# Optimization experiments

Measured on AMD Instinct MI355X. Metric: run time of the kernel, lower is better.

The kernel has to match this reference:

```python
import jax, jax.numpy as jnp
import numpy as np

CLASS_NUM = 12
ROWS, COLS = 3, 4
ALPHA = 0.6

def _att_values():
    # attention_lst[i][j] = 1 / (# of 8-connected neighbors of cell i in the
    # ROWSxCOLS stimulus grid); note it is independent of j.
    i = np.arange(CLASS_NUM)
    r, c = i // COLS, i % COLS
    up, dn = (r - 1 >= 0), (r + 1 <= ROWS - 1)
    lf, rt = (c - 1 >= 0), (c + 1 <= COLS - 1)
    cnt = (up.astype(np.int32) + dn + lf + rt
           + (up & lf) + (up & rt) + (dn & lf) + (dn & rt))
    return (1.0 / cnt).astype(np.float32)

_ATT = jnp.asarray(_att_values())  # [CLASS_NUM]

def setup_inputs() -> dict:
    key = jax.random.key(0)
    k1, k2 = jax.random.split(key)
    B = 4194304
    outputs = jax.random.normal(k1, (B, CLASS_NUM), dtype=jnp.float32)
    targets = jax.random.randint(k2, (B,), 0, CLASS_NUM, dtype=jnp.int64)
    return {"outputs": outputs, "targets": targets}

def reference(outputs, targets):
    B = outputs.shape[0]
    logp = jax.nn.log_softmax(outputs, axis=1)          # [B, C]
    row_sum = jnp.sum(logp, axis=1)                     # [B]
    logp_t = jnp.take_along_axis(logp, targets[:, None], axis=1)[:, 0]  # [B]
    att = _ATT[targets]                                  # [B], row-constant label value
    # smoothed row = att everywhere, 1.0 at target =>
    # sum(logp * smoothed) = att * (row_sum - logp_t) + logp_t
    att_loss = -jnp.mean(att * (row_sum - logp_t) + logp_t)
    ce_loss = -jnp.mean(logp_t)
    return ALPHA * ce_loss + (1.0 - ALPHA) * att_loss
```

## Files before the change

### kernel.cpp

```cpp
#include <hip/hip_runtime.h>


#define CLS 12
#define ALPHA_F 0.6f

__device__ __constant__ float ATT_TAB[CLS] = {
    1.0f/3.0f, 1.0f/5.0f, 1.0f/5.0f, 1.0f/3.0f,
    1.0f/5.0f, 1.0f/8.0f, 1.0f/8.0f, 1.0f/5.0f,
    1.0f/3.0f, 1.0f/5.0f, 1.0f/5.0f, 1.0f/3.0f
};

__global__ __launch_bounds__(256)
void ce_marginal_smooth_kernel(const float* __restrict__ outputs,
                               const int*   __restrict__ targets,
                               float* __restrict__ out,
                               int B, float inv_b)
{
    const int tid    = blockIdx.x * blockDim.x + threadIdx.x;
    const int stride = gridDim.x * blockDim.x;

    float acc = 0.0f;

    for (int row = tid; row < B; row += stride) {
        const float4* p = reinterpret_cast<const float4*>(outputs) + (size_t)row * 3;
        float4 f0 = p[0];
        float4 f1 = p[1];
        float4 f2 = p[2];
        float x[CLS] = { f0.x, f0.y, f0.z, f0.w,
                         f1.x, f1.y, f1.z, f1.w,
                         f2.x, f2.y, f2.z, f2.w };

        float m = x[0];
        #pragma unroll
        for (int j = 1; j < CLS; ++j) m = fmaxf(m, x[j]);

        float se = 0.0f, rs = 0.0f;
        #pragma unroll
        for (int j = 0; j < CLS; ++j) {
            se += __expf(x[j] - m);
            rs += x[j];
        }
        float lse = m + __logf(se);

        int t = targets[row];
        float xt = x[0];
        #pragma unroll
        for (int j = 1; j < CLS; ++j) xt = (t == j) ? x[j] : xt;

        float logp_t  = xt - lse;
        float row_sum = rs - (float)CLS * lse;
        float att     = ATT_TAB[t];

        float v = -ALPHA_F * logp_t
                  - (1.0f - ALPHA_F) * (att * (row_sum - logp_t) + logp_t);
        acc += v;
    }

    acc *= inv_b;

    #pragma unroll
    for (int off = 32; off > 0; off >>= 1)
        acc += __shfl_down(acc, off, 64);

    if ((threadIdx.x & 63) == 0)
        atomicAdd(out, acc);
}

extern "C" void kernel_launch(void* const* d_in, const int* in_sizes, int n_in,
                              void* d_out, int out_size, void* d_ws, size_t ws_size,
                              hipStream_t stream)
{
    const float* outputs = (const float*)d_in[0];
    const int*   targets = (const int*)d_in[1];
    float*       out     = (float*)d_out;

    const int B = in_sizes[1];
    const float inv_b = 1.0f / (float)B;

    hipMemsetAsync(out, 0, sizeof(float), stream);

    const int block = 256;
    const int grid  = 1024;
    ce_marginal_smooth_kernel<<<grid, block, 0, stream>>>(outputs, targets, out, B, inv_b);
}
```

Before: 319.5 us.

## Stage row tiles through LDS for coalesced loads and use two-pass reduction

Each block now loads 256 rows as contiguous float4s, with consecutive threads reading consecutive addresses, and stages them in shared memory. Each thread then reads back its own 48-byte row. This replaces the earlier per-thread strided 3x float4 loads, which coalesced poorly. The grid-stride loop with 1024 blocks becomes one row per thread across many blocks. The atomic plus memset are replaced by per-block partials in the workspace and a single-block final reduction kernel. The costs are an extra kernel launch, an LDS round trip with possible bank conflicts on the 3-float4 stride reads, and losing multi-row amortisation per thread.

```diff
diff --git a/kernel.cpp b/kernel.cpp
--- a/kernel.cpp
+++ b/kernel.cpp
@@ -3,6 +3,7 @@
 
 #define CLS 12
 #define ALPHA_F 0.6f
+#define ROWS_PER_BLOCK 256
 
 __device__ __constant__ float ATT_TAB[CLS] = {
     1.0f/3.0f, 1.0f/5.0f, 1.0f/5.0f, 1.0f/3.0f,
@@ -11,21 +12,43 @@
 };
 
 __global__ __launch_bounds__(256)
-void ce_marginal_smooth_kernel(const float* __restrict__ outputs,
-                               const int*   __restrict__ targets,
-                               float* __restrict__ out,
-                               int B, float inv_b)
+void ce_ms_partial_kernel(const float* __restrict__ outputs,
+                          const int*   __restrict__ targets,
+                          float* __restrict__ partial,
+                          int B, float inv_b)
 {
-    const int tid    = blockIdx.x * blockDim.x + threadIdx.x;
-    const int stride = gridDim.x * blockDim.x;
+    __shared__ float tile[ROWS_PER_BLOCK * CLS];
+    __shared__ float warp_part[4];
+
+    const int t = threadIdx.x;
+    const int row0 = blockIdx.x * ROWS_PER_BLOCK;
+    const long long f4_base = (long long)row0 * 3;
+    const long long f4_total = (long long)B * 3;
+
+    const float4* gp = reinterpret_cast<const float4*>(outputs);
+    float4 v0, v1, v2;
+    {
+        long long g0 = f4_base + t;
+        long long g1 = f4_base + t + 256;
+        long long g2 = f4_base + t + 512;
+        v0 = (g0 < f4_total) ? gp[g0] : make_float4(0.f, 0.f, 0.f, 0.f);
+        v1 = (g1 < f4_total) ? gp[g1] : make_float4(0.f, 0.f, 0.f, 0.f);
+        v2 = (g2 < f4_total) ? gp[g2] : make_float4(0.f, 0.f, 0.f, 0.f);
+    }
+    const int my_row = row0 + t;
+    const int tgt = (my_row < B) ? targets[my_row] : 0;
+
+    float4* tp = reinterpret_cast<float4*>(tile);
+    tp[t]       = v0;
+    tp[t + 256] = v1;
+    tp[t + 512] = v2;
+    __syncthreads();
 
     float acc = 0.0f;
-
-    for (int row = tid; row < B; row += stride) {
-        const float4* p = reinterpret_cast<const float4*>(outputs) + (size_t)row * 3;
-        float4 f0 = p[0];
-        float4 f1 = p[1];
-        float4 f2 = p[2];
+    if (my_row < B) {
+        float4 f0 = tp[t * 3 + 0];
+        float4 f1 = tp[t * 3 + 1];
+        float4 f2 = tp[t * 3 + 2];
         float x[CLS] = { f0.x, f0.y, f0.z, f0.w,
                          f1.x, f1.y, f1.z, f1.w,
                          f2.x, f2.y, f2.z, f2.w };
@@ -42,28 +65,52 @@
         }
         float lse = m + __logf(se);
 
-        int t = targets[row];
         float xt = x[0];
         #pragma unroll
-        for (int j = 1; j < CLS; ++j) xt = (t == j) ? x[j] : xt;
+        for (int j = 1; j < CLS; ++j) xt = (tgt == j) ? x[j] : xt;
 
         float logp_t  = xt - lse;
         float row_sum = rs - (float)CLS * lse;
-        float att     = ATT_TAB[t];
+        float att     = ATT_TAB[tgt];
 
-        float v = -ALPHA_F * logp_t
-                  - (1.0f - ALPHA_F) * (att * (row_sum - logp_t) + logp_t);
-        acc += v;
+        acc = (-ALPHA_F * logp_t
+               - (1.0f - ALPHA_F) * (att * (row_sum - logp_t) + logp_t)) * inv_b;
     }
-
-    acc *= inv_b;
 
     #pragma unroll
     for (int off = 32; off > 0; off >>= 1)
         acc += __shfl_down(acc, off, 64);
 
-    if ((threadIdx.x & 63) == 0)
-        atomicAdd(out, acc);
+    const int wave = t >> 6;
+    if ((t & 63) == 0) warp_part[wave] = acc;
+    __syncthreads();
+    if (t == 0)
+        partial[blockIdx.x] = warp_part[0] + warp_part[1] + warp_part[2] + warp_part[3];
+}
+
+__global__ __launch_bounds__(256)
+void ce_ms_final_kernel(const float* __restrict__ partial, float* __restrict__ out, int n)
+{
+    const int t = threadIdx.x;
+    float a0 = 0.f, a1 = 0.f, a2 = 0.f, a3 = 0.f;
+    for (int i = t; i < n; i += 1024) {
+        a0 += partial[i];
+        if (i + 256 < n) a1 += partial[i + 256];
+        if (i + 512 < n) a2 += partial[i + 512];
+        if (i + 768 < n) a3 += partial[i + 768];
+    }
+    float acc = (a0 + a1) + (a2 + a3);
+
+    #pragma unroll
+    for (int off = 32; off > 0; off >>= 1)
+        acc += __shfl_down(acc, off, 64);
+
+    __shared__ float warp_part[4];
+    const int wave = t >> 6;
+    if ((t & 63) == 0) warp_part[wave] = acc;
+    __syncthreads();
+    if (t == 0)
+        out[0] = warp_part[0] + warp_part[1] + warp_part[2] + warp_part[3];
 }
 
 extern "C" void kernel_launch(void* const* d_in, const int* in_sizes, int n_in,
@@ -73,13 +120,12 @@
     const float* outputs = (const float*)d_in[0];
     const int*   targets = (const int*)d_in[1];
     float*       out     = (float*)d_out;
+    float*       partial = (float*)d_ws;
 
     const int B = in_sizes[1];
     const float inv_b = 1.0f / (float)B;
 
-    hipMemsetAsync(out, 0, sizeof(float), stream);
-
-    const int block = 256;
-    const int grid  = 1024;
-    ce_marginal_smooth_kernel<<<grid, block, 0, stream>>>(outputs, targets, out, B, inv_b);
+    const int grid = (B + ROWS_PER_BLOCK - 1) / ROWS_PER_BLOCK;
+    ce_ms_partial_kernel<<<grid, 256, 0, stream>>>(outputs, targets, partial, B, inv_b);
+    ce_ms_final_kernel<<<1, 256, 0, stream>>>(partial, out, grid);
 }
```

Measured after the change: 290.6 us. 9.0% less time.
